# Optimization experiments

Measured on AMD Instinct MI355X. Metric: run time of the kernel, lower is better.

The kernel has to match this reference:

```python
import jax, jax.numpy as jnp
import numpy as np

MSL, BS, ENC = 64, 128, 1024
HID, EMB, ATOM = 512, 50, 64
MAX_STEPS = 50
SOS = 1


def setup_inputs() -> dict:
    key = jax.random.key(0)
    ks = jax.random.split(key, 14)
    s = 0.05
    emb = jax.random.normal(ks[1], (ATOM, EMB), jnp.float32) * s
    emb = emb.at[0].set(0.0)  # padding_idx=0
    return {
        'encoder_output': jax.random.normal(ks[0], (MSL, BS, ENC), jnp.float32),
        'emb': emb,
        'w_h0': jax.random.normal(ks[2], (2 * HID, ENC), jnp.float32) * s,
        'b_h0': jax.random.normal(ks[3], (2 * HID,), jnp.float32) * s,
        'w_ih0': jax.random.normal(ks[4], (3 * HID, EMB), jnp.float32) * s,
        'w_hh0': jax.random.normal(ks[5], (3 * HID, HID), jnp.float32) * s,
        'b_ih0': jax.random.normal(ks[6], (3 * HID,), jnp.float32) * s,
        'b_hh0': jax.random.normal(ks[7], (3 * HID,), jnp.float32) * s,
        'w_ih1': jax.random.normal(ks[8], (3 * HID, HID), jnp.float32) * s,
        'w_hh1': jax.random.normal(ks[9], (3 * HID, HID), jnp.float32) * s,
        'b_ih1': jax.random.normal(ks[10], (3 * HID,), jnp.float32) * s,
        'b_hh1': jax.random.normal(ks[11], (3 * HID,), jnp.float32) * s,
        'w_out': jax.random.normal(ks[12], (ATOM, HID), jnp.float32) * s,
        'b_out': jax.random.normal(ks[13], (ATOM,), jnp.float32) * s,
    }


def _gru_cell(x, h, w_ih, w_hh, b_ih, b_hh):
    gi = x @ w_ih.T + b_ih          # [B, 3H]
    gh = h @ w_hh.T + b_hh          # [B, 3H]
    i_r, i_z, i_n = jnp.split(gi, 3, axis=-1)
    h_r, h_z, h_n = jnp.split(gh, 3, axis=-1)
    r = jax.nn.sigmoid(i_r + h_r)
    z = jax.nn.sigmoid(i_z + h_z)
    n = jnp.tanh(i_n + r * h_n)
    return (1.0 - z) * n + z * h


def reference(encoder_output, emb, w_h0, b_h0, w_ih0, w_hh0, b_ih0, b_hh0,
              w_ih1, w_hh1, b_ih1, b_hh1, w_out, b_out):
    msl, bs, _ = encoder_output.shape
    B = msl * bs
    H = w_hh0.shape[1]
    # encoder_to_h0: Linear + Tanh -> [B, 2, H] -> [2, B, H]
    h = jnp.tanh(encoder_output.reshape(B, -1) @ w_h0.T + b_h0)
    h = h.reshape(B, 2, H).transpose(1, 0, 2)
    h0, h1 = h[0], h[1]
    e = jnp.broadcast_to(emb[SOS], (B, emb.shape[1]))  # SOS embedding

    def step(carry, _):
        h0, h1, e = carry
        h0 = _gru_cell(e, h0, w_ih0, w_hh0, b_ih0, b_hh0)
        h1 = _gru_cell(h0, h1, w_ih1, w_hh1, b_ih1, b_hh1)
        y = jax.nn.log_softmax(h1 @ w_out.T + b_out, axis=-1)  # [B, A]
        p = jnp.argmax(y, axis=-1)
        e = emb[p]
        return (h0, h1, e), y

    _, Y = jax.lax.scan(step, (h0, h1, e), None, length=MAX_STEPS)
    return Y.reshape(MAX_STEPS, msl, bs, -1)[:-1]
```

## Files before the change

### kernel.cpp

```cpp
#include <hip/hip_runtime.h>
#include <hip/hip_bf16.h>
#include <cstdint>
#include <cstddef>


typedef __attribute__((ext_vector_type(8))) __bf16 bf16x8;
typedef __attribute__((ext_vector_type(4))) __bf16 bf16x4;
typedef __attribute__((ext_vector_type(4))) float f32x4;

#define B_ROWS 8192
#define HID 512
#define GATE3 1536
#define ATOM 64
#define NSTEP 49

#define GLOAD_LDS16(gp, sp)                                                   \
  __builtin_amdgcn_global_load_lds(                                           \
      (__attribute__((address_space(1))) void*)(gp),                          \
      (__attribute__((address_space(3))) void*)(sp), 16, 0, 0)

#define PROLOGUE_FENCE()                                                      \
  do {                                                                        \
    __builtin_amdgcn_sched_barrier(0);                                        \
    asm volatile("" ::: "memory");                                            \
  } while (0)

__device__ inline float sig_(float x) { return 1.f / (1.f + __expf(-x)); }
__device__ inline float tanh_(float x) { return 2.f / (1.f + __expf(-2.f * x)) - 1.f; }

__global__ __launch_bounds__(256) void gru0_step(
    const __bf16* __restrict__ h0b_c, const __bf16* __restrict__ whh0f,
    const float* __restrict__ G0p, const int* __restrict__ p,
    const float* __restrict__ bhh0p,
    const float* __restrict__ h0f_c, float* __restrict__ h0f_n,
    __bf16* __restrict__ h0b_n)
{
    __shared__ __bf16 As[2][64 * 32];

    const int tid = threadIdx.x, lane = tid & 63, w = tid >> 6;
    const int u = lane & 15, q = lane >> 4;
    const int m0 = blockIdx.x * 64;
    const int t_ = blockIdx.y * 4 + w;
    const int j  = t_ * 16 + u;
    const int qb = t_ * 48 + u;
    const int k0   = (q ^ ((u >> 1) & 3)) * 8;
    const int scol = ((tid & 3) ^ ((tid >> 3) & 3)) * 8;
    const int wo = w * 512;

    const __bf16* Ap = h0b_c + (size_t)(m0 + (tid >> 2)) * HID + scol;
    const __bf16* Bf = whh0f + (size_t)(t_ * 48) * 512 + lane * 8;
    #define BFR0(g, kt) (*(const bf16x8*)(Bf + (size_t)((g) * 16 + (kt)) * 512))

    f32x4 acc[4][3] = {};
    bf16x8 bfr[2][3];

    GLOAD_LDS16(Ap, &As[0][wo]); Ap += 32;
    bfr[0][0] = BFR0(0, 0);
    bfr[0][1] = BFR0(1, 0);
    bfr[0][2] = BFR0(2, 0);
    PROLOGUE_FENCE();

    #pragma unroll
    for (int kt = 0; kt < 16; ++kt) {
        const int cur = kt & 1;
        if (kt < 15) {
            GLOAD_LDS16(Ap, &As[cur ^ 1][wo]); Ap += 32;
            bfr[cur ^ 1][0] = BFR0(0, kt + 1);
            bfr[cur ^ 1][1] = BFR0(1, kt + 1);
            bfr[cur ^ 1][2] = BFR0(2, kt + 1);
            if (kt == 0) asm volatile("s_waitcnt vmcnt(0)" ::: "memory");
            else         asm volatile("s_waitcnt vmcnt(4)" ::: "memory");
        } else {
            asm volatile("s_waitcnt vmcnt(0)" ::: "memory");
        }
        __builtin_amdgcn_s_barrier();

        bf16x8 af[4];
        #pragma unroll
        for (int mf = 0; mf < 4; ++mf)
            af[mf] = *(const bf16x8*)&As[cur][(mf * 16 + u) * 32 + k0];
        #pragma unroll
        for (int mf = 0; mf < 4; ++mf)
            #pragma unroll
            for (int g = 0; g < 3; ++g)
                acc[mf][g] = __builtin_amdgcn_mfma_f32_16x16x32_bf16(
                    af[mf], bfr[cur][g], acc[mf][g], 0, 0, 0);

        asm volatile("s_waitcnt lgkmcnt(0)" ::: "memory");
        __builtin_amdgcn_s_barrier();
    }

    const float bhr = bhh0p[qb], bhz = bhh0p[qb + 16], bhn = bhh0p[qb + 32];
    const int rbase = m0 + (q << 2);
    #pragma unroll
    for (int mf = 0; mf < 4; ++mf)
        #pragma unroll
        for (int r = 0; r < 4; ++r) {
            const int row = rbase + mf * 16 + r;
            const float* g0 = G0p + (size_t)p[row] * GATE3 + qb;
            const float rr = sig_(g0[0]  + acc[mf][0][r] + bhr);
            const float zz = sig_(g0[16] + acc[mf][1][r] + bhz);
            const float nn = tanh_(g0[32] + rr * (acc[mf][2][r] + bhn));
            const float hp = h0f_c[(size_t)row * HID + j];
            const float hv = (1.f - zz) * nn + zz * hp;
            h0f_n[(size_t)row * HID + j] = hv;
            h0b_n[(size_t)row * HID + j] = (__bf16)hv;
        }
}

__global__ __launch_bounds__(256) void gru1_fused(
    const __bf16* __restrict__ h0b_n, const __bf16* __restrict__ wih1f,
    const __bf16* __restrict__ h1b_c, const __bf16* __restrict__ whh1f,
    const float* __restrict__ bih1p, const float* __restrict__ bhh1p,
    const float* __restrict__ h1f_c, float* __restrict__ h1f_n,
    __bf16* __restrict__ h1b_n)
{
    __shared__ __bf16 Asi[2][64 * 32];
    __shared__ __bf16 Ash[2][64 * 32];

    const int tid = threadIdx.x, lane = tid & 63, w = tid >> 6;
    const int u = lane & 15, q = lane >> 4;
    const int m0 = blockIdx.x * 64;
    const int t_ = blockIdx.y * 4 + w;
    const int j  = t_ * 16 + u;
    const int qb = t_ * 48 + u;
    const int k0   = (q ^ ((u >> 1) & 3)) * 8;
    const int scol = ((tid & 3) ^ ((tid >> 3) & 3)) * 8;
    const int wo = w * 512;

    const __bf16* Api = h0b_n + (size_t)(m0 + (tid >> 2)) * HID + scol;
    const __bf16* Aph = h1b_c + (size_t)(m0 + (tid >> 2)) * HID + scol;
    const __bf16* Bfi = wih1f + (size_t)(t_ * 48) * 512 + lane * 8;
    const __bf16* Bfh = whh1f + (size_t)(t_ * 48) * 512 + lane * 8;
    #define BFRI(g, kt) (*(const bf16x8*)(Bfi + (size_t)((g) * 16 + (kt)) * 512))
    #define BFRH(g, kt) (*(const bf16x8*)(Bfh + (size_t)((g) * 16 + (kt)) * 512))

    f32x4 acc_i[4][3] = {};
    f32x4 acc_h[4][3] = {};
    bf16x8 bfi[2][3], bfh[2][3];

    GLOAD_LDS16(Api, &Asi[0][wo]); Api += 32;
    GLOAD_LDS16(Aph, &Ash[0][wo]); Aph += 32;
    #pragma unroll
    for (int g = 0; g < 3; ++g) {
        bfi[0][g] = BFRI(g, 0);
        bfh[0][g] = BFRH(g, 0);
    }
    PROLOGUE_FENCE();

    #pragma unroll
    for (int kt = 0; kt < 16; ++kt) {
        const int cur = kt & 1;
        if (kt < 15) {
            GLOAD_LDS16(Api, &Asi[cur ^ 1][wo]); Api += 32;
            GLOAD_LDS16(Aph, &Ash[cur ^ 1][wo]); Aph += 32;
            #pragma unroll
            for (int g = 0; g < 3; ++g) {
                bfi[cur ^ 1][g] = BFRI(g, kt + 1);
                bfh[cur ^ 1][g] = BFRH(g, kt + 1);
            }
            if (kt == 0) asm volatile("s_waitcnt vmcnt(0)" ::: "memory");
            else         asm volatile("s_waitcnt vmcnt(8)" ::: "memory");
        } else {
            asm volatile("s_waitcnt vmcnt(0)" ::: "memory");
        }
        __builtin_amdgcn_s_barrier();

        #pragma unroll
        for (int mf = 0; mf < 4; ++mf) {
            const bf16x8 afi = *(const bf16x8*)&Asi[cur][(mf * 16 + u) * 32 + k0];
            #pragma unroll
            for (int g = 0; g < 3; ++g)
                acc_i[mf][g] = __builtin_amdgcn_mfma_f32_16x16x32_bf16(
                    afi, bfi[cur][g], acc_i[mf][g], 0, 0, 0);
            const bf16x8 afh = *(const bf16x8*)&Ash[cur][(mf * 16 + u) * 32 + k0];
            #pragma unroll
            for (int g = 0; g < 3; ++g)
                acc_h[mf][g] = __builtin_amdgcn_mfma_f32_16x16x32_bf16(
                    afh, bfh[cur][g], acc_h[mf][g], 0, 0, 0);
        }

        asm volatile("s_waitcnt lgkmcnt(0)" ::: "memory");
        __builtin_amdgcn_s_barrier();
    }

    const float bir = bih1p[qb], biz = bih1p[qb + 16], bin = bih1p[qb + 32];
    const float bhr = bhh1p[qb], bhz = bhh1p[qb + 16], bhn = bhh1p[qb + 32];
    const int rbase = m0 + (q << 2);
    #pragma unroll
    for (int mf = 0; mf < 4; ++mf)
        #pragma unroll
        for (int r = 0; r < 4; ++r) {
            const int row = rbase + mf * 16 + r;
            const float rr = sig_(acc_i[mf][0][r] + bir + acc_h[mf][0][r] + bhr);
            const float zz = sig_(acc_i[mf][1][r] + biz + acc_h[mf][1][r] + bhz);
            const float nn = tanh_(acc_i[mf][2][r] + bin +
                                   rr * (acc_h[mf][2][r] + bhn));
            const float hp = h1f_c[(size_t)row * HID + j];
            const float hv = (1.f - zz) * nn + zz * hp;
            h1f_n[(size_t)row * HID + j] = hv;
            h1b_n[(size_t)row * HID + j] = (__bf16)hv;
        }
}

__global__ __launch_bounds__(128) void out_mfma(
    const __bf16* __restrict__ h1b, const __bf16* __restrict__ woutf,
    const float* __restrict__ bout, float* __restrict__ y, int* __restrict__ p)
{
    __shared__ __bf16 As[2][32 * 32];

    const int tid  = threadIdx.x;
    const int lane = tid & 63;
    const int w    = tid >> 6;
    const int m0   = blockIdx.x * 32;
    const int u    = lane & 15, q = lane >> 4;
    const int k0   = (q ^ ((u >> 1) & 3)) * 8;
    const int scol = ((tid & 3) ^ ((tid >> 3) & 3)) * 8;
    const int wo   = w * 512;

    f32x4 acc[4] = {};
    bf16x8 bfr[2][4];

    const __bf16* Ap = h1b + (size_t)(m0 + (tid >> 2)) * HID + scol;
    const __bf16* Bf = woutf + lane * 8;
    #define BFRW(nf, kt) (*(const bf16x8*)(Bf + (size_t)((nf) * 16 + (kt)) * 512))

    GLOAD_LDS16(Ap, &As[0][wo]); Ap += 32;
    #pragma unroll
    for (int nf = 0; nf < 4; ++nf) bfr[0][nf] = BFRW(nf, 0);
    PROLOGUE_FENCE();

    #pragma unroll
    for (int kt = 0; kt < 16; ++kt) {
        const int cur = kt & 1;
        if (kt < 15) {
            GLOAD_LDS16(Ap, &As[cur ^ 1][wo]); Ap += 32;
            #pragma unroll
            for (int nf = 0; nf < 4; ++nf) bfr[cur ^ 1][nf] = BFRW(nf, kt + 1);
            if (kt == 0) asm volatile("s_waitcnt vmcnt(0)" ::: "memory");
            else         asm volatile("s_waitcnt vmcnt(5)" ::: "memory");
        } else {
            asm volatile("s_waitcnt vmcnt(0)" ::: "memory");
        }
        __builtin_amdgcn_s_barrier();

        const bf16x8 af = *(const bf16x8*)&As[cur][(w * 16 + u) * 32 + k0];
        #pragma unroll
        for (int nf = 0; nf < 4; ++nf)
            acc[nf] = __builtin_amdgcn_mfma_f32_16x16x32_bf16(
                af, bfr[cur][nf], acc[nf], 0, 0, 0);

        asm volatile("s_waitcnt lgkmcnt(0)" ::: "memory");
        __builtin_amdgcn_s_barrier();
    }

    #pragma unroll
    for (int r = 0; r < 4; ++r) {
        const int row = m0 + w * 16 + (q << 2) + r;
        float l[4];
        #pragma unroll
        for (int nf = 0; nf < 4; ++nf) l[nf] = acc[nf][r] + bout[nf * 16 + u];

        float mv = l[0]; int mi = u;
        #pragma unroll
        for (int nf = 1; nf < 4; ++nf)
            if (l[nf] > mv) { mv = l[nf]; mi = nf * 16 + u; }
        #pragma unroll
        for (int off = 1; off <= 8; off <<= 1) {
            const float ov = __shfl_xor(mv, off, 64);
            const int   oi = __shfl_xor(mi, off, 64);
            if (ov > mv || (ov == mv && oi < mi)) { mv = ov; mi = oi; }
        }
        float se = 0.f;
        #pragma unroll
        for (int nf = 0; nf < 4; ++nf) se += __expf(l[nf] - mv);
        #pragma unroll
        for (int off = 1; off <= 8; off <<= 1) se += __shfl_xor(se, off, 64);
        const float lse = logf(se);

        #pragma unroll
        for (int nf = 0; nf < 4; ++nf)
            y[(size_t)row * ATOM + nf * 16 + u] = l[nf] - mv - lse;
        if (u == 0) p[row] = mi;
    }
}

__global__ __launch_bounds__(256) void gemm_init(
    const __bf16* __restrict__ A, const __bf16* __restrict__ B,
    int N, int K, const float* __restrict__ bias,
    float* __restrict__ H0f, __bf16* __restrict__ H0b,
    float* __restrict__ H1f, __bf16* __restrict__ H1b)
{
    __shared__ __bf16 As[128 * 32];
    __shared__ __bf16 Bs[128 * 32];

    const int tid  = threadIdx.x;
    const int lane = tid & 63;
    const int w    = tid >> 6;
    const int wm   = w >> 1, wn = w & 1;
    const int m0   = blockIdx.x * 128;
    const int n0   = blockIdx.y * 128;

    f32x4 acc[4][4] = {};

    const int i0 = w * 64 + lane;
    const int i1 = i0 + 256;
    const __bf16* Ap0 = A + (size_t)(m0 + (i0 >> 2)) * K + (i0 & 3) * 8;
    const __bf16* Ap1 = A + (size_t)(m0 + (i1 >> 2)) * K + (i1 & 3) * 8;
    const __bf16* Bp0 = B + (size_t)(n0 + (i0 >> 2)) * K + (i0 & 3) * 8;
    const __bf16* Bp1 = B + (size_t)(n0 + (i1 >> 2)) * K + (i1 & 3) * 8;
    __bf16* As0 = As + w * 512;
    __bf16* As1 = As + 2048 + w * 512;
    __bf16* Bs0 = Bs + w * 512;
    __bf16* Bs1 = Bs + 2048 + w * 512;

    const int mrow = wm * 64 + (lane & 15);
    const int nrow = wn * 64 + (lane & 15);
    const int koff = (lane >> 4) * 8;

    for (int kt = 0; kt < K / 32; ++kt) {
        __syncthreads();
        GLOAD_LDS16(Ap0, As0);
        GLOAD_LDS16(Ap1, As1);
        GLOAD_LDS16(Bp0, Bs0);
        GLOAD_LDS16(Bp1, Bs1);
        Ap0 += 32; Ap1 += 32; Bp0 += 32; Bp1 += 32;
        __syncthreads();

        bf16x8 af[4], bfr[4];
        #pragma unroll
        for (int f = 0; f < 4; ++f) {
            af[f]  = *(const bf16x8*)&As[(mrow + f * 16) * 32 + koff];
            bfr[f] = *(const bf16x8*)&Bs[(nrow + f * 16) * 32 + koff];
        }
        #pragma unroll
        for (int mf = 0; mf < 4; ++mf)
            #pragma unroll
            for (int nf = 0; nf < 4; ++nf)
                acc[mf][nf] = __builtin_amdgcn_mfma_f32_16x16x32_bf16(
                    af[mf], bfr[nf], acc[mf][nf], 0, 0, 0);
    }

    const int colb = n0 + wn * 64 + (lane & 15);
    const int rowb = m0 + wm * 64 + ((lane >> 4) << 2);
    #pragma unroll
    for (int mf = 0; mf < 4; ++mf)
        #pragma unroll
        for (int nf = 0; nf < 4; ++nf) {
            const int col = colb + nf * 16;
            #pragma unroll
            for (int r = 0; r < 4; ++r) {
                const int row = rowb + mf * 16 + r;
                const float v = tanhf(acc[mf][nf][r] + bias[col]);
                if (col < HID) {
                    H0f[(size_t)row * HID + col] = v;
                    H0b[(size_t)row * HID + col] = (__bf16)v;
                } else {
                    H1f[(size_t)row * HID + col - HID] = v;
                    H1b[(size_t)row * HID + col - HID] = (__bf16)v;
                }
            }
        }
}

__device__ inline int permQ(int q) {
    const int t = q / 48, rem = q % 48;
    return (rem / 16) * HID + t * 16 + (rem % 16);
}

__device__ inline size_t fragOff(int r, int k) {
    return (size_t)((r >> 4) * 16 + (k >> 5)) * 512 +
           ((k >> 3) & 3) * 128 + (r & 15) * 8 + (k & 7);
}

__global__ __launch_bounds__(256) void f2b(const float* __restrict__ s,
                                           __bf16* __restrict__ d, int n)
{
    const int i = (blockIdx.x * 256 + threadIdx.x) * 4;
    if (i + 3 < n) {
        const float4 v = *(const float4*)(s + i);
        bf16x4 o = { (__bf16)v.x, (__bf16)v.y, (__bf16)v.z, (__bf16)v.w };
        *(bf16x4*)(d + i) = o;
    }
}

__global__ __launch_bounds__(256) void f2bpf(const float* __restrict__ s,
                                             __bf16* __restrict__ d)
{
    const int idx = blockIdx.x * 256 + threadIdx.x;
    const int q = idx >> 7, k4 = (idx & 127) << 2;
    const int o = permQ(q);
    const float4 v = *(const float4*)(s + (size_t)o * HID + k4);
    bf16x4 ov = { (__bf16)v.x, (__bf16)v.y, (__bf16)v.z, (__bf16)v.w };
    *(bf16x4*)(d + fragOff(q, k4)) = ov;
}

__global__ __launch_bounds__(256) void f2bf(const float* __restrict__ s,
                                            __bf16* __restrict__ d)
{
    const int idx = blockIdx.x * 256 + threadIdx.x;
    if (idx >= ATOM * 128) return;
    const int r = idx >> 7, k4 = (idx & 127) << 2;
    const float4 v = *(const float4*)(s + (size_t)r * HID + k4);
    bf16x4 ov = { (__bf16)v.x, (__bf16)v.y, (__bf16)v.z, (__bf16)v.w };
    *(bf16x4*)(d + fragOff(r, k4)) = ov;
}

__global__ __launch_bounds__(256) void bperm(const float* __restrict__ s,
                                             float* __restrict__ d)
{
    const int q = blockIdx.x * 256 + threadIdx.x;
    if (q < GATE3) d[q] = s[permQ(q)];
}

__global__ __launch_bounds__(256) void g0pk(const float* __restrict__ emb,
                                            const float* __restrict__ wih0,
                                            const float* __restrict__ bih0,
                                            float* __restrict__ G0p)
{
    const int i = blockIdx.x * 256 + threadIdx.x;
    if (i >= ATOM * GATE3) return;
    const int a = i / GATE3, q = i % GATE3;
    const int o = permQ(q);
    float s = bih0[o];
    for (int k = 0; k < 50; ++k) s += emb[a * 50 + k] * wih0[o * 50 + k];
    G0p[i] = s;
}

__global__ __launch_bounds__(256) void initp(int* __restrict__ p)
{
    const int i = blockIdx.x * 256 + threadIdx.x;
    if (i < B_ROWS) p[i] = 1;
}

extern "C" void kernel_launch(void* const* d_in, const int* in_sizes, int n_in,
                              void* d_out, int out_size, void* d_ws, size_t ws_size,
                              hipStream_t stream)
{
    (void)in_sizes; (void)n_in; (void)out_size; (void)ws_size;
    const float* enc   = (const float*)d_in[0];
    const float* emb   = (const float*)d_in[1];
    const float* w_h0  = (const float*)d_in[2];
    const float* b_h0  = (const float*)d_in[3];
    const float* w_ih0 = (const float*)d_in[4];
    const float* w_hh0 = (const float*)d_in[5];
    const float* b_ih0 = (const float*)d_in[6];
    const float* b_hh0 = (const float*)d_in[7];
    const float* w_ih1 = (const float*)d_in[8];
    const float* w_hh1 = (const float*)d_in[9];
    const float* b_ih1 = (const float*)d_in[10];
    const float* b_hh1 = (const float*)d_in[11];
    const float* w_out = (const float*)d_in[12];
    const float* b_out = (const float*)d_in[13];
    float* out = (float*)d_out;

    char* ws = (char*)d_ws;
    size_t off = 0;
    auto alloc = [&](size_t bytes) -> void* {
        void* pp = ws + off;
        off = (off + bytes + 255) & ~(size_t)255;
        return pp;
    };
    __bf16* whh0f = (__bf16*)alloc((size_t)GATE3 * HID * 2);
    __bf16* wih1f = (__bf16*)alloc((size_t)GATE3 * HID * 2);
    __bf16* whh1f = (__bf16*)alloc((size_t)GATE3 * HID * 2);
    __bf16* woutf = (__bf16*)alloc((size_t)ATOM * HID * 2);
    float*  G0p   = (float*) alloc((size_t)ATOM * GATE3 * 4);
    float*  bhh0p = (float*) alloc(GATE3 * 4);
    float*  bih1p = (float*) alloc(GATE3 * 4);
    float*  bhh1p = (float*) alloc(GATE3 * 4);
    float*  h0f[2]; __bf16* h0b[2]; float* h1f[2]; __bf16* h1b[2];
    for (int i = 0; i < 2; ++i) {
        h0f[i] = (float*) alloc((size_t)B_ROWS * HID * 4);
        h0b[i] = (__bf16*)alloc((size_t)B_ROWS * HID * 2);
        h1f[i] = (float*) alloc((size_t)B_ROWS * HID * 4);
        h1b[i] = (__bf16*)alloc((size_t)B_ROWS * HID * 2);
    }
    int* p = (int*)alloc((size_t)B_ROWS * 4);
    __bf16* enc_b = (__bf16*)alloc((size_t)B_ROWS * 1024 * 2);
    __bf16* wh0b  = (__bf16*)alloc((size_t)1024 * 1024 * 2);

    f2b  <<<8192, 256, 0, stream>>>(enc,  enc_b, B_ROWS * 1024);
    f2b  <<<1024, 256, 0, stream>>>(w_h0, wh0b,  1024 * 1024);
    f2bf <<<32,   256, 0, stream>>>(w_out, woutf);
    f2bpf<<<768,  256, 0, stream>>>(w_hh0, whh0f);
    f2bpf<<<768,  256, 0, stream>>>(w_ih1, wih1f);
    f2bpf<<<768,  256, 0, stream>>>(w_hh1, whh1f);
    bperm<<<6, 256, 0, stream>>>(b_hh0, bhh0p);
    bperm<<<6, 256, 0, stream>>>(b_ih1, bih1p);
    bperm<<<6, 256, 0, stream>>>(b_hh1, bhh1p);
    g0pk<<<384, 256, 0, stream>>>(emb, w_ih0, b_ih0, G0p);
    initp<<<32, 256, 0, stream>>>(p);

    gemm_init<<<dim3(B_ROWS / 128, 1024 / 128), 256, 0, stream>>>(
        enc_b, wh0b, 1024, 1024, b_h0, h0f[0], h0b[0], h1f[0], h1b[0]);

    const dim3 gGrid(B_ROWS / 64, GATE3 / 192);
    for (int step = 0; step < NSTEP; ++step) {
        const int cur = step & 1, nxt = cur ^ 1;
        gru0_step<<<gGrid, 256, 0, stream>>>(
            h0b[cur], whh0f, G0p, p, bhh0p, h0f[cur], h0f[nxt], h0b[nxt]);
        gru1_fused<<<gGrid, 256, 0, stream>>>(
            h0b[nxt], wih1f, h1b[cur], whh1f, bih1p, bhh1p,
            h1f[cur], h1f[nxt], h1b[nxt]);
        out_mfma<<<B_ROWS / 32, 128, 0, stream>>>(
            h1b[nxt], woutf, b_out, out + (size_t)step * B_ROWS * ATOM, p);
    }
}
```

Baseline: 3.832 ms.

## Fuse all decode steps into one persistent kernel with LDS-resident hidden state

Replaces the three kernels launched per step (GRU layer 0, GRU layer 1, output projection with log-softmax) with a single persistent kernel. Each block owns 32 rows and keeps their fp32 h0/h1 state in swizzled LDS for all 49 steps, converting to bf16 when building MFMA operands. This removes about 150 launches and the per-step global round trips of hidden state and argmax indices. In exchange, every block streams the full recurrent weight matrices from cache each step with no explicit prefetch, so the smaller 32-row tile halves weight reuse compared with the old 64-row tiles. The roughly 134 KB LDS footprint also limits occupancy to one block per CU.

```diff
diff --git a/kernel.cpp b/kernel.cpp
--- a/kernel.cpp
+++ b/kernel.cpp
@@ -13,275 +13,222 @@
 #define GATE3 1536
 #define ATOM 64
 #define NSTEP 49
+#define LROW 524
 
 #define GLOAD_LDS16(gp, sp)                                                   \
   __builtin_amdgcn_global_load_lds(                                           \
       (__attribute__((address_space(1))) void*)(gp),                          \
       (__attribute__((address_space(3))) void*)(sp), 16, 0, 0)
 
-#define PROLOGUE_FENCE()                                                      \
-  do {                                                                        \
-    __builtin_amdgcn_sched_barrier(0);                                        \
-    asm volatile("" ::: "memory");                                            \
-  } while (0)
-
 __device__ inline float sig_(float x) { return 1.f / (1.f + __expf(-x)); }
 __device__ inline float tanh_(float x) { return 2.f / (1.f + __expf(-2.f * x)) - 1.f; }
 
-__global__ __launch_bounds__(256) void gru0_step(
-    const __bf16* __restrict__ h0b_c, const __bf16* __restrict__ whh0f,
-    const float* __restrict__ G0p, const int* __restrict__ p,
+__device__ __forceinline__ int lof(int row, int c) {
+    return row * LROW + (((c >> 3) ^ (row & 7)) << 3) + (c & 7);
+}
+
+__device__ __forceinline__ bf16x8 ldsA(const float* hs, int row, int kt, int q) {
+    const int g = ((kt << 2) + q) ^ (row & 7);
+    const float* p0 = &hs[row * LROW + (g << 3)];
+    const float4 a = *(const float4*)p0;
+    const float4 b = *(const float4*)(p0 + 4);
+    bf16x8 r;
+    r[0] = (__bf16)a.x; r[1] = (__bf16)a.y; r[2] = (__bf16)a.z; r[3] = (__bf16)a.w;
+    r[4] = (__bf16)b.x; r[5] = (__bf16)b.y; r[6] = (__bf16)b.z; r[7] = (__bf16)b.w;
+    return r;
+}
+
+__global__ __launch_bounds__(512, 2) void decode_fused(
+    const float* __restrict__ h0f_g, const float* __restrict__ h1f_g,
+    const __bf16* __restrict__ whh0f, const float* __restrict__ G0p,
     const float* __restrict__ bhh0p,
-    const float* __restrict__ h0f_c, float* __restrict__ h0f_n,
-    __bf16* __restrict__ h0b_n)
-{
-    __shared__ __bf16 As[2][64 * 32];
+    const __bf16* __restrict__ wih1f, const __bf16* __restrict__ whh1f,
+    const float* __restrict__ bih1p, const float* __restrict__ bhh1p,
+    const __bf16* __restrict__ woutf, const float* __restrict__ bout,
+    float* __restrict__ y)
+{
+    __shared__ float h0s[32 * LROW];
+    __shared__ float h1s[32 * LROW];
+    __shared__ int   p_s[32];
 
     const int tid = threadIdx.x, lane = tid & 63, w = tid >> 6;
     const int u = lane & 15, q = lane >> 4;
-    const int m0 = blockIdx.x * 64;
-    const int t_ = blockIdx.y * 4 + w;
-    const int j  = t_ * 16 + u;
-    const int qb = t_ * 48 + u;
-    const int k0   = (q ^ ((u >> 1) & 3)) * 8;
-    const int scol = ((tid & 3) ^ ((tid >> 3) & 3)) * 8;
-    const int wo = w * 512;
-
-    const __bf16* Ap = h0b_c + (size_t)(m0 + (tid >> 2)) * HID + scol;
-    const __bf16* Bf = whh0f + (size_t)(t_ * 48) * 512 + lane * 8;
-    #define BFR0(g, kt) (*(const bf16x8*)(Bf + (size_t)((g) * 16 + (kt)) * 512))
-
-    f32x4 acc[4][3] = {};
-    bf16x8 bfr[2][3];
-
-    GLOAD_LDS16(Ap, &As[0][wo]); Ap += 32;
-    bfr[0][0] = BFR0(0, 0);
-    bfr[0][1] = BFR0(1, 0);
-    bfr[0][2] = BFR0(2, 0);
-    PROLOGUE_FENCE();
-
+    const int m0 = blockIdx.x * 32;
+
+    for (int idx = tid; idx < 32 * 128; idx += 512) {
+        const int row = idx >> 7, c0 = (idx & 127) << 2;
+        const int off = row * LROW + (((c0 >> 3) ^ (row & 7)) << 3) + (c0 & 7);
+        *(float4*)&h0s[off] = *(const float4*)&h0f_g[(size_t)(m0 + row) * HID + c0];
+        *(float4*)&h1s[off] = *(const float4*)&h1f_g[(size_t)(m0 + row) * HID + c0];
+    }
+    if (tid < 32) p_s[tid] = 1;
+
+    const size_t wbase = (size_t)(w * 192) * HID + (size_t)lane * 8;
+    const __bf16* B0 = whh0f + wbase;
+    const __bf16* Bi = wih1f + wbase;
+    const __bf16* Bh = whh1f + wbase;
+    const __bf16* Bw = woutf + (size_t)lane * 8;
+
+    float bh0r[4], bh0z[4], bh0n[4];
+    float b1r[4], b1z[4], b1in[4], b1hn[4];
     #pragma unroll
-    for (int kt = 0; kt < 16; ++kt) {
-        const int cur = kt & 1;
-        if (kt < 15) {
-            GLOAD_LDS16(Ap, &As[cur ^ 1][wo]); Ap += 32;
-            bfr[cur ^ 1][0] = BFR0(0, kt + 1);
-            bfr[cur ^ 1][1] = BFR0(1, kt + 1);
-            bfr[cur ^ 1][2] = BFR0(2, kt + 1);
-            if (kt == 0) asm volatile("s_waitcnt vmcnt(0)" ::: "memory");
-            else         asm volatile("s_waitcnt vmcnt(4)" ::: "memory");
-        } else {
-            asm volatile("s_waitcnt vmcnt(0)" ::: "memory");
+    for (int tr = 0; tr < 4; ++tr) {
+        const int qb = (w * 4 + tr) * 48 + u;
+        bh0r[tr] = bhh0p[qb]; bh0z[tr] = bhh0p[qb + 16]; bh0n[tr] = bhh0p[qb + 32];
+        b1r[tr]  = bih1p[qb] + bhh1p[qb];
+        b1z[tr]  = bih1p[qb + 16] + bhh1p[qb + 16];
+        b1in[tr] = bih1p[qb + 32];
+        b1hn[tr] = bhh1p[qb + 32];
+    }
+    float bo[4] = {0.f, 0.f, 0.f, 0.f};
+    if (w < 2) {
+        #pragma unroll
+        for (int nf = 0; nf < 4; ++nf) bo[nf] = bout[nf * 16 + u];
+    }
+    __syncthreads();
+
+    for (int step = 0; step < NSTEP; ++step) {
+        {
+            f32x4 acc0[2][4][3] = {};
+            #pragma unroll 4
+            for (int kt = 0; kt < 16; ++kt) {
+                const bf16x8 a0 = ldsA(h0s, u, kt, q);
+                const bf16x8 a1 = ldsA(h0s, u + 16, kt, q);
+                #pragma unroll
+                for (int tr = 0; tr < 4; ++tr)
+                    #pragma unroll
+                    for (int g = 0; g < 3; ++g) {
+                        const bf16x8 bf = *(const bf16x8*)(B0 + (size_t)(tr * 48 + g * 16 + kt) * HID);
+                        acc0[0][tr][g] = __builtin_amdgcn_mfma_f32_16x16x32_bf16(a0, bf, acc0[0][tr][g], 0, 0, 0);
+                        acc0[1][tr][g] = __builtin_amdgcn_mfma_f32_16x16x32_bf16(a1, bf, acc0[1][tr][g], 0, 0, 0);
+                    }
+            }
+            __syncthreads();
+
+            int pv[2][4];
+            #pragma unroll
+            for (int mf = 0; mf < 2; ++mf)
+                #pragma unroll
+                for (int r = 0; r < 4; ++r) pv[mf][r] = p_s[mf * 16 + q * 4 + r];
+
+            #pragma unroll
+            for (int mf = 0; mf < 2; ++mf)
+                #pragma unroll
+                for (int tr = 0; tr < 4; ++tr) {
+                    const int j  = (w * 4 + tr) * 16 + u;
+                    const int qb = (w * 4 + tr) * 48 + u;
+                    #pragma unroll
+                    for (int r = 0; r < 4; ++r) {
+                        const int row = mf * 16 + q * 4 + r;
+                        const float* g0 = G0p + (size_t)pv[mf][r] * GATE3 + qb;
+                        const float rr = sig_(g0[0]  + acc0[mf][tr][0][r] + bh0r[tr]);
+                        const float zz = sig_(g0[16] + acc0[mf][tr][1][r] + bh0z[tr]);
+                        const float nn = tanh_(g0[32] + rr * (acc0[mf][tr][2][r] + bh0n[tr]));
+                        const int o = lof(row, j);
+                        h0s[o] = (1.f - zz) * nn + zz * h0s[o];
+                    }
+                }
         }
-        __builtin_amdgcn_s_barrier();
-
-        bf16x8 af[4];
-        #pragma unroll
-        for (int mf = 0; mf < 4; ++mf)
-            af[mf] = *(const bf16x8*)&As[cur][(mf * 16 + u) * 32 + k0];
-        #pragma unroll
-        for (int mf = 0; mf < 4; ++mf)
-            #pragma unroll
-            for (int g = 0; g < 3; ++g)
-                acc[mf][g] = __builtin_amdgcn_mfma_f32_16x16x32_bf16(
-                    af[mf], bfr[cur][g], acc[mf][g], 0, 0, 0);
-
-        asm volatile("s_waitcnt lgkmcnt(0)" ::: "memory");
-        __builtin_amdgcn_s_barrier();
-    }
-
-    const float bhr = bhh0p[qb], bhz = bhh0p[qb + 16], bhn = bhh0p[qb + 32];
-    const int rbase = m0 + (q << 2);
-    #pragma unroll
-    for (int mf = 0; mf < 4; ++mf)
-        #pragma unroll
-        for (int r = 0; r < 4; ++r) {
-            const int row = rbase + mf * 16 + r;
-            const float* g0 = G0p + (size_t)p[row] * GATE3 + qb;
-            const float rr = sig_(g0[0]  + acc[mf][0][r] + bhr);
-            const float zz = sig_(g0[16] + acc[mf][1][r] + bhz);
-            const float nn = tanh_(g0[32] + rr * (acc[mf][2][r] + bhn));
-            const float hp = h0f_c[(size_t)row * HID + j];
-            const float hv = (1.f - zz) * nn + zz * hp;
-            h0f_n[(size_t)row * HID + j] = hv;
-            h0b_n[(size_t)row * HID + j] = (__bf16)hv;
+        __syncthreads();
+
+        {
+            f32x4 ai[2][4][3] = {};
+            #pragma unroll 4
+            for (int kt = 0; kt < 16; ++kt) {
+                const bf16x8 a0 = ldsA(h0s, u, kt, q);
+                const bf16x8 a1 = ldsA(h0s, u + 16, kt, q);
+                #pragma unroll
+                for (int tr = 0; tr < 4; ++tr)
+                    #pragma unroll
+                    for (int g = 0; g < 3; ++g) {
+                        const bf16x8 bf = *(const bf16x8*)(Bi + (size_t)(tr * 48 + g * 16 + kt) * HID);
+                        ai[0][tr][g] = __builtin_amdgcn_mfma_f32_16x16x32_bf16(a0, bf, ai[0][tr][g], 0, 0, 0);
+                        ai[1][tr][g] = __builtin_amdgcn_mfma_f32_16x16x32_bf16(a1, bf, ai[1][tr][g], 0, 0, 0);
+                    }
+            }
+            f32x4 an[2][4] = {};
+            #pragma unroll 4
+            for (int kt = 0; kt < 16; ++kt) {
+                const bf16x8 a0 = ldsA(h1s, u, kt, q);
+                const bf16x8 a1 = ldsA(h1s, u + 16, kt, q);
+                #pragma unroll
+                for (int tr = 0; tr < 4; ++tr) {
+                    const bf16x8 br = *(const bf16x8*)(Bh + (size_t)(tr * 48 + 0 * 16 + kt) * HID);
+                    ai[0][tr][0] = __builtin_amdgcn_mfma_f32_16x16x32_bf16(a0, br, ai[0][tr][0], 0, 0, 0);
+                    ai[1][tr][0] = __builtin_amdgcn_mfma_f32_16x16x32_bf16(a1, br, ai[1][tr][0], 0, 0, 0);
+                    const bf16x8 bz = *(const bf16x8*)(Bh + (size_t)(tr * 48 + 1 * 16 + kt) * HID);
+                    ai[0][tr][1] = __builtin_amdgcn_mfma_f32_16x16x32_bf16(a0, bz, ai[0][tr][1], 0, 0, 0);
+                    ai[1][tr][1] = __builtin_amdgcn_mfma_f32_16x16x32_bf16(a1, bz, ai[1][tr][1], 0, 0, 0);
+                    const bf16x8 bn = *(const bf16x8*)(Bh + (size_t)(tr * 48 + 2 * 16 + kt) * HID);
+                    an[0][tr] = __builtin_amdgcn_mfma_f32_16x16x32_bf16(a0, bn, an[0][tr], 0, 0, 0);
+                    an[1][tr] = __builtin_amdgcn_mfma_f32_16x16x32_bf16(a1, bn, an[1][tr], 0, 0, 0);
+                }
+            }
+            __syncthreads();
+
+            #pragma unroll
+            for (int mf = 0; mf < 2; ++mf)
+                #pragma unroll
+                for (int tr = 0; tr < 4; ++tr) {
+                    const int j = (w * 4 + tr) * 16 + u;
+                    #pragma unroll
+                    for (int r = 0; r < 4; ++r) {
+                        const int row = mf * 16 + q * 4 + r;
+                        const float rr = sig_(ai[mf][tr][0][r] + b1r[tr]);
+                        const float zz = sig_(ai[mf][tr][1][r] + b1z[tr]);
+                        const float nn = tanh_(ai[mf][tr][2][r] + b1in[tr] +
+                                               rr * (an[mf][tr][r] + b1hn[tr]));
+                        const int o = lof(row, j);
+                        h1s[o] = (1.f - zz) * nn + zz * h1s[o];
+                    }
+                }
         }
-}
-
-__global__ __launch_bounds__(256) void gru1_fused(
-    const __bf16* __restrict__ h0b_n, const __bf16* __restrict__ wih1f,
-    const __bf16* __restrict__ h1b_c, const __bf16* __restrict__ whh1f,
-    const float* __restrict__ bih1p, const float* __restrict__ bhh1p,
-    const float* __restrict__ h1f_c, float* __restrict__ h1f_n,
-    __bf16* __restrict__ h1b_n)
-{
-    __shared__ __bf16 Asi[2][64 * 32];
-    __shared__ __bf16 Ash[2][64 * 32];
-
-    const int tid = threadIdx.x, lane = tid & 63, w = tid >> 6;
-    const int u = lane & 15, q = lane >> 4;
-    const int m0 = blockIdx.x * 64;
-    const int t_ = blockIdx.y * 4 + w;
-    const int j  = t_ * 16 + u;
-    const int qb = t_ * 48 + u;
-    const int k0   = (q ^ ((u >> 1) & 3)) * 8;
-    const int scol = ((tid & 3) ^ ((tid >> 3) & 3)) * 8;
-    const int wo = w * 512;
-
-    const __bf16* Api = h0b_n + (size_t)(m0 + (tid >> 2)) * HID + scol;
-    const __bf16* Aph = h1b_c + (size_t)(m0 + (tid >> 2)) * HID + scol;
-    const __bf16* Bfi = wih1f + (size_t)(t_ * 48) * 512 + lane * 8;
-    const __bf16* Bfh = whh1f + (size_t)(t_ * 48) * 512 + lane * 8;
-    #define BFRI(g, kt) (*(const bf16x8*)(Bfi + (size_t)((g) * 16 + (kt)) * 512))
-    #define BFRH(g, kt) (*(const bf16x8*)(Bfh + (size_t)((g) * 16 + (kt)) * 512))
-
-    f32x4 acc_i[4][3] = {};
-    f32x4 acc_h[4][3] = {};
-    bf16x8 bfi[2][3], bfh[2][3];
-
-    GLOAD_LDS16(Api, &Asi[0][wo]); Api += 32;
-    GLOAD_LDS16(Aph, &Ash[0][wo]); Aph += 32;
-    #pragma unroll
-    for (int g = 0; g < 3; ++g) {
-        bfi[0][g] = BFRI(g, 0);
-        bfh[0][g] = BFRH(g, 0);
-    }
-    PROLOGUE_FENCE();
-
-    #pragma unroll
-    for (int kt = 0; kt < 16; ++kt) {
-        const int cur = kt & 1;
-        if (kt < 15) {
-            GLOAD_LDS16(Api, &Asi[cur ^ 1][wo]); Api += 32;
-            GLOAD_LDS16(Aph, &Ash[cur ^ 1][wo]); Aph += 32;
-            #pragma unroll
-            for (int g = 0; g < 3; ++g) {
-                bfi[cur ^ 1][g] = BFRI(g, kt + 1);
-                bfh[cur ^ 1][g] = BFRH(g, kt + 1);
-            }
-            if (kt == 0) asm volatile("s_waitcnt vmcnt(0)" ::: "memory");
-            else         asm volatile("s_waitcnt vmcnt(8)" ::: "memory");
-        } else {
-            asm volatile("s_waitcnt vmcnt(0)" ::: "memory");
+        __syncthreads();
+
+        if (w < 2) {
+            f32x4 aq[4] = {};
+            #pragma unroll 4
+            for (int kt = 0; kt < 16; ++kt) {
+                const bf16x8 af = ldsA(h1s, w * 16 + u, kt, q);
+                #pragma unroll
+                for (int nf = 0; nf < 4; ++nf) {
+                    const bf16x8 bf = *(const bf16x8*)(Bw + (size_t)(nf * 16 + kt) * HID);
+                    aq[nf] = __builtin_amdgcn_mfma_f32_16x16x32_bf16(af, bf, aq[nf], 0, 0, 0);
+                }
+            }
+            float* ystep = y + (size_t)step * B_ROWS * ATOM;
+            #pragma unroll
+            for (int r = 0; r < 4; ++r) {
+                const int lr = w * 16 + q * 4 + r;
+                float l[4];
+                #pragma unroll
+                for (int nf = 0; nf < 4; ++nf) l[nf] = aq[nf][r] + bo[nf];
+
+                float mv = l[0]; int mi = u;
+                #pragma unroll
+                for (int nf = 1; nf < 4; ++nf)
+                    if (l[nf] > mv) { mv = l[nf]; mi = nf * 16 + u; }
+                #pragma unroll
+                for (int off = 1; off <= 8; off <<= 1) {
+                    const float ov = __shfl_xor(mv, off, 64);
+                    const int   oi = __shfl_xor(mi, off, 64);
+                    if (ov > mv || (ov == mv && oi < mi)) { mv = ov; mi = oi; }
+                }
+                float se = 0.f;
+                #pragma unroll
+                for (int nf = 0; nf < 4; ++nf) se += __expf(l[nf] - mv);
+                #pragma unroll
+                for (int off = 1; off <= 8; off <<= 1) se += __shfl_xor(se, off, 64);
+                const float lse = logf(se);
+
+                float* yrow = ystep + (size_t)(m0 + lr) * ATOM;
+                #pragma unroll
+                for (int nf = 0; nf < 4; ++nf)
+                    yrow[nf * 16 + u] = l[nf] - mv - lse;
+                if (u == 0) p_s[lr] = mi;
+            }
         }
-        __builtin_amdgcn_s_barrier();
-
-        #pragma unroll
-        for (int mf = 0; mf < 4; ++mf) {
-            const bf16x8 afi = *(const bf16x8*)&Asi[cur][(mf * 16 + u) * 32 + k0];
-            #pragma unroll
-            for (int g = 0; g < 3; ++g)
-                acc_i[mf][g] = __builtin_amdgcn_mfma_f32_16x16x32_bf16(
-                    afi, bfi[cur][g], acc_i[mf][g], 0, 0, 0);
-            const bf16x8 afh = *(const bf16x8*)&Ash[cur][(mf * 16 + u) * 32 + k0];
-            #pragma unroll
-            for (int g = 0; g < 3; ++g)
-                acc_h[mf][g] = __builtin_amdgcn_mfma_f32_16x16x32_bf16(
-                    afh, bfh[cur][g], acc_h[mf][g], 0, 0, 0);
-        }
-
-        asm volatile("s_waitcnt lgkmcnt(0)" ::: "memory");
-        __builtin_amdgcn_s_barrier();
-    }
-
-    const float bir = bih1p[qb], biz = bih1p[qb + 16], bin = bih1p[qb + 32];
-    const float bhr = bhh1p[qb], bhz = bhh1p[qb + 16], bhn = bhh1p[qb + 32];
-    const int rbase = m0 + (q << 2);
-    #pragma unroll
-    for (int mf = 0; mf < 4; ++mf)
-        #pragma unroll
-        for (int r = 0; r < 4; ++r) {
-            const int row = rbase + mf * 16 + r;
-            const float rr = sig_(acc_i[mf][0][r] + bir + acc_h[mf][0][r] + bhr);
-            const float zz = sig_(acc_i[mf][1][r] + biz + acc_h[mf][1][r] + bhz);
-            const float nn = tanh_(acc_i[mf][2][r] + bin +
-                                   rr * (acc_h[mf][2][r] + bhn));
-            const float hp = h1f_c[(size_t)row * HID + j];
-            const float hv = (1.f - zz) * nn + zz * hp;
-            h1f_n[(size_t)row * HID + j] = hv;
-            h1b_n[(size_t)row * HID + j] = (__bf16)hv;
-        }
-}
-
-__global__ __launch_bounds__(128) void out_mfma(
-    const __bf16* __restrict__ h1b, const __bf16* __restrict__ woutf,
-    const float* __restrict__ bout, float* __restrict__ y, int* __restrict__ p)
-{
-    __shared__ __bf16 As[2][32 * 32];
-
-    const int tid  = threadIdx.x;
-    const int lane = tid & 63;
-    const int w    = tid >> 6;
-    const int m0   = blockIdx.x * 32;
-    const int u    = lane & 15, q = lane >> 4;
-    const int k0   = (q ^ ((u >> 1) & 3)) * 8;
-    const int scol = ((tid & 3) ^ ((tid >> 3) & 3)) * 8;
-    const int wo   = w * 512;
-
-    f32x4 acc[4] = {};
-    bf16x8 bfr[2][4];
-
-    const __bf16* Ap = h1b + (size_t)(m0 + (tid >> 2)) * HID + scol;
-    const __bf16* Bf = woutf + lane * 8;
-    #define BFRW(nf, kt) (*(const bf16x8*)(Bf + (size_t)((nf) * 16 + (kt)) * 512))
-
-    GLOAD_LDS16(Ap, &As[0][wo]); Ap += 32;
-    #pragma unroll
-    for (int nf = 0; nf < 4; ++nf) bfr[0][nf] = BFRW(nf, 0);
-    PROLOGUE_FENCE();
-
-    #pragma unroll
-    for (int kt = 0; kt < 16; ++kt) {
-        const int cur = kt & 1;
-        if (kt < 15) {
-            GLOAD_LDS16(Ap, &As[cur ^ 1][wo]); Ap += 32;
-            #pragma unroll
-            for (int nf = 0; nf < 4; ++nf) bfr[cur ^ 1][nf] = BFRW(nf, kt + 1);
-            if (kt == 0) asm volatile("s_waitcnt vmcnt(0)" ::: "memory");
-            else         asm volatile("s_waitcnt vmcnt(5)" ::: "memory");
-        } else {
-            asm volatile("s_waitcnt vmcnt(0)" ::: "memory");
-        }
-        __builtin_amdgcn_s_barrier();
-
-        const bf16x8 af = *(const bf16x8*)&As[cur][(w * 16 + u) * 32 + k0];
-        #pragma unroll
-        for (int nf = 0; nf < 4; ++nf)
-            acc[nf] = __builtin_amdgcn_mfma_f32_16x16x32_bf16(
-                af, bfr[cur][nf], acc[nf], 0, 0, 0);
-
-        asm volatile("s_waitcnt lgkmcnt(0)" ::: "memory");
-        __builtin_amdgcn_s_barrier();
-    }
-
-    #pragma unroll
-    for (int r = 0; r < 4; ++r) {
-        const int row = m0 + w * 16 + (q << 2) + r;
-        float l[4];
-        #pragma unroll
-        for (int nf = 0; nf < 4; ++nf) l[nf] = acc[nf][r] + bout[nf * 16 + u];
-
-        float mv = l[0]; int mi = u;
-        #pragma unroll
-        for (int nf = 1; nf < 4; ++nf)
-            if (l[nf] > mv) { mv = l[nf]; mi = nf * 16 + u; }
-        #pragma unroll
-        for (int off = 1; off <= 8; off <<= 1) {
-            const float ov = __shfl_xor(mv, off, 64);
-            const int   oi = __shfl_xor(mi, off, 64);
-            if (ov > mv || (ov == mv && oi < mi)) { mv = ov; mi = oi; }
-        }
-        float se = 0.f;
-        #pragma unroll
-        for (int nf = 0; nf < 4; ++nf) se += __expf(l[nf] - mv);
-        #pragma unroll
-        for (int off = 1; off <= 8; off <<= 1) se += __shfl_xor(se, off, 64);
-        const float lse = logf(se);
-
-        #pragma unroll
-        for (int nf = 0; nf < 4; ++nf)
-            y[(size_t)row * ATOM + nf * 16 + u] = l[nf] - mv - lse;
-        if (u == 0) p[row] = mi;
+        __syncthreads();
     }
 }
 
@@ -425,12 +372,6 @@
     float s = bih0[o];
     for (int k = 0; k < 50; ++k) s += emb[a * 50 + k] * wih0[o * 50 + k];
     G0p[i] = s;
-}
-
-__global__ __launch_bounds__(256) void initp(int* __restrict__ p)
-{
-    const int i = blockIdx.x * 256 + threadIdx.x;
-    if (i < B_ROWS) p[i] = 1;
 }
 
 extern "C" void kernel_launch(void* const* d_in, const int* in_sizes, int n_in,
@@ -469,14 +410,10 @@
     float*  bhh0p = (float*) alloc(GATE3 * 4);
     float*  bih1p = (float*) alloc(GATE3 * 4);
     float*  bhh1p = (float*) alloc(GATE3 * 4);
-    float*  h0f[2]; __bf16* h0b[2]; float* h1f[2]; __bf16* h1b[2];
-    for (int i = 0; i < 2; ++i) {
-        h0f[i] = (float*) alloc((size_t)B_ROWS * HID * 4);
-        h0b[i] = (__bf16*)alloc((size_t)B_ROWS * HID * 2);
-        h1f[i] = (float*) alloc((size_t)B_ROWS * HID * 4);
-        h1b[i] = (__bf16*)alloc((size_t)B_ROWS * HID * 2);
-    }
-    int* p = (int*)alloc((size_t)B_ROWS * 4);
+    float*  h0f = (float*) alloc((size_t)B_ROWS * HID * 4);
+    __bf16* h0b = (__bf16*)alloc((size_t)B_ROWS * HID * 2);
+    float*  h1f = (float*) alloc((size_t)B_ROWS * HID * 4);
+    __bf16* h1b = (__bf16*)alloc((size_t)B_ROWS * HID * 2);
     __bf16* enc_b = (__bf16*)alloc((size_t)B_ROWS * 1024 * 2);
     __bf16* wh0b  = (__bf16*)alloc((size_t)1024 * 1024 * 2);
 
@@ -490,20 +427,12 @@
     bperm<<<6, 256, 0, stream>>>(b_ih1, bih1p);
     bperm<<<6, 256, 0, stream>>>(b_hh1, bhh1p);
     g0pk<<<384, 256, 0, stream>>>(emb, w_ih0, b_ih0, G0p);
-    initp<<<32, 256, 0, stream>>>(p);
 
     gemm_init<<<dim3(B_ROWS / 128, 1024 / 128), 256, 0, stream>>>(
-        enc_b, wh0b, 1024, 1024, b_h0, h0f[0], h0b[0], h1f[0], h1b[0]);
-
-    const dim3 gGrid(B_ROWS / 64, GATE3 / 192);
-    for (int step = 0; step < NSTEP; ++step) {
-        const int cur = step & 1, nxt = cur ^ 1;
-        gru0_step<<<gGrid, 256, 0, stream>>>(
-            h0b[cur], whh0f, G0p, p, bhh0p, h0f[cur], h0f[nxt], h0b[nxt]);
-        gru1_fused<<<gGrid, 256, 0, stream>>>(
-            h0b[nxt], wih1f, h1b[cur], whh1f, bih1p, bhh1p,
-            h1f[cur], h1f[nxt], h1b[nxt]);
-        out_mfma<<<B_ROWS / 32, 128, 0, stream>>>(
-            h1b[nxt], woutf, b_out, out + (size_t)step * B_ROWS * ATOM, p);
-    }
-}
+        enc_b, wh0b, 1024, 1024, b_h0, h0f, h0b, h1f, h1b);
+
+    decode_fused<<<256, 512, 0, stream>>>(
+        h0f, h1f, whh0f, G0p, bhh0p,
+        wih1f, whh1f, bih1p, bhh1p,
+        woutf, b_out, out);
+}
```

After: 8.515 ms. 2.22x slower.
